# Optimization experiments

Hardware: AMD Instinct MI355X
Metric: run time of the kernel (lower is better)

Reference implementation:

```python
import jax, jax.numpy as jnp
import numpy as np

B, N, T, D = 8, 32, 49, 4
K = 4            # edge_types
HE = 256         # encoder_hidden
HD = 256         # decoder_hidden (msg_hid == msg_out == n_hid)
TEMP = 0.5
SKIP_FIRST = True
EPS = 1e-5
E = N * (N - 1)  # 992 directed edges (off-diagonal)


def setup_inputs() -> dict:
    key = jax.random.key(0)
    ks = jax.random.split(key, 32)
    it = iter(range(32))

    def lin(fi, fo):
        k = ks[next(it)]
        return (jax.random.normal(k, (fi, fo), jnp.float32) / np.sqrt(fi)).astype(jnp.float32)

    def bias(fo):
        return jnp.full((fo,), 0.1, jnp.float32)

    off = ~np.eye(N, dtype=bool)
    recv_np, send_np = np.where(off)  # rel_rec rows, rel_send cols
    recv_idx = jnp.asarray(recv_np, jnp.int32)
    send_idx = jnp.asarray(send_np, jnp.int32)

    data = jax.random.normal(ks[next(it)], (B, N, T, D), jnp.float32)
    u = jax.random.uniform(ks[next(it)], (B, E, K), jnp.float32, 1e-6, 1.0 - 1e-6)
    gumbel = -jnp.log(-jnp.log(u))

    inp = {"data": data, "gumbel": gumbel, "recv_idx": recv_idx, "send_idx": send_idx}
    # Encoder: 4 MLPs (fc1, fc2, bn gamma/beta) + fc_out
    enc_dims = [(T * D, HE), (2 * HE, HE), (HE, HE), (3 * HE, HE)]
    for i, (fi, fh) in enumerate(enc_dims, start=1):
        inp[f"e{i}_w1"] = lin(fi, HE)
        inp[f"e{i}_b1"] = bias(HE)
        inp[f"e{i}_w2"] = lin(HE, HE)
        inp[f"e{i}_b2"] = bias(HE)
        inp[f"e{i}_g"] = jnp.ones((HE,), jnp.float32)
        inp[f"e{i}_be"] = jnp.zeros((HE,), jnp.float32)
    inp["fc_w"] = lin(HE, K)
    inp["fc_b"] = bias(K)
    # Decoder: per-edge-type message MLPs (stacked) + output MLP
    inp["mw1"] = jnp.stack([lin(2 * D, HD) for _ in range(K)])
    inp["mb1"] = jnp.zeros((K, HD), jnp.float32)
    inp["mw2"] = jnp.stack([lin(HD, HD) for _ in range(K)])
    inp["mb2"] = jnp.zeros((K, HD), jnp.float32)
    inp["ow1"] = lin(D + HD, HD)
    inp["ob1"] = jnp.zeros((HD,), jnp.float32)
    inp["ow2"] = lin(HD, HD)
    inp["ob2"] = jnp.zeros((HD,), jnp.float32)
    inp["ow3"] = lin(HD, D)
    inp["ob3"] = jnp.zeros((D,), jnp.float32)
    return inp


def _mlp(x, w1, b1, w2, b2, g, be):
    # Two-layer ELU net + batch norm over all leading dims (training-mode stats).
    x = jax.nn.elu(x @ w1 + b1)
    x = jax.nn.elu(x @ w2 + b2)
    m = x.mean(axis=(0, 1), keepdims=True)
    v = x.var(axis=(0, 1), keepdims=True)
    return (x - m) / jnp.sqrt(v + EPS) * g + be


def reference(data, gumbel, recv_idx, send_idx,
              e1_w1, e1_b1, e1_w2, e1_b2, e1_g, e1_be,
              e2_w1, e2_b1, e2_w2, e2_b2, e2_g, e2_be,
              e3_w1, e3_b1, e3_w2, e3_b2, e3_g, e3_be,
              e4_w1, e4_b1, e4_w2, e4_b2, e4_g, e4_be,
              fc_w, fc_b, mw1, mb1, mw2, mb2,
              ow1, ob1, ow2, ob2, ow3, ob3):
    # ---------- Encoder ----------
    x = data.reshape(B, N, T * D)
    x = _mlp(x, e1_w1, e1_b1, e1_w2, e1_b2, e1_g, e1_be)          # [B,N,HE]
    edges = jnp.concatenate([x[:, send_idx], x[:, recv_idx]], -1)  # [B,E,2HE]
    x = _mlp(edges, e2_w1, e2_b1, e2_w2, e2_b2, e2_g, e2_be)       # [B,E,HE]
    x_skip = x
    # edge2node: rel_rec^T @ x == scatter-add by receiver, then /N
    incoming = jnp.zeros((B, N, HE), x.dtype).at[:, recv_idx, :].add(x) / N
    x = _mlp(incoming, e3_w1, e3_b1, e3_w2, e3_b2, e3_g, e3_be)    # [B,N,HE]
    edges2 = jnp.concatenate([x[:, send_idx], x[:, recv_idx]], -1)  # [B,E,2HE]
    x = jnp.concatenate([edges2, x_skip], -1)                       # [B,E,3HE]
    x = _mlp(x, e4_w1, e4_b1, e4_w2, e4_b2, e4_g, e4_be)
    logits = x @ fc_w + fc_b                                        # [B,E,K]

    rel_type = jax.nn.softmax((logits + gumbel) / TEMP, axis=-1)    # gumbel-softmax (soft)
    prob = jax.nn.softmax(logits, axis=-1)

    # ---------- Decoder (pred_steps=1) ----------
    inputs = jnp.transpose(data, (0, 2, 1, 3))                      # [B,T,N,D]
    rt = rel_type[:, None, :, :]                                    # [B,1,E,K] broadcast over T
    senders = inputs[:, :, send_idx, :]                             # [B,T,E,D]
    receivers = inputs[:, :, recv_idx, :]
    pre_msg = jnp.concatenate([senders, receivers], -1)             # [B,T,E,2D]

    start = 1 if SKIP_FIRST else 0
    all_msgs = jnp.zeros((B, T, E, HD), pre_msg.dtype)
    for k in range(start, K):
        msg = jax.nn.relu(pre_msg @ mw1[k] + mb1[k])
        msg = jax.nn.relu(msg @ mw2[k] + mb2[k])
        all_msgs = all_msgs + msg * rt[..., k:k + 1]

    # scatter-sum messages to receiving nodes
    agg = jnp.zeros((B, T, N, HD), all_msgs.dtype).at[:, :, recv_idx, :].add(all_msgs)
    aug = jnp.concatenate([inputs, agg], -1)                        # [B,T,N,D+HD]
    p = jax.nn.relu(aug @ ow1 + ob1)
    p = jax.nn.relu(p @ ow2 + ob2)
    p = p @ ow3 + ob3
    step = inputs + p                                               # [B,T,N,D]

    output = jnp.transpose(step[:, :T - 1], (0, 2, 1, 3))           # [B,N,T-1,D]
    return (output, prob)
```

## Files before the change

kernel.cpp:

```cpp
#include <hip/hip_runtime.h>
#include <hip/hip_bf16.h>

#define NNODES 32
#define TSTEPS 49
#define NEDGE  992
#define ROWS_E 7936
#define ROWS_OUT 12544
#define EPSV 1e-5f

typedef __hip_bfloat16 bf16;
typedef __attribute__((ext_vector_type(8))) short bf16x8;
typedef __attribute__((ext_vector_type(4))) float f32x4;

__device__ inline float eluf(float x){ return x > 0.f ? x : (__expf(x) - 1.f); }
__device__ inline float bfu2f(unsigned short u){ unsigned v = ((unsigned)u) << 16; return *reinterpret_cast<float*>(&v); }
__device__ inline unsigned pack_bf16(float a, float b){
  __hip_bfloat16 ha = __float2bfloat16(a), hb = __float2bfloat16(b);
  unsigned short ua = *reinterpret_cast<unsigned short*>(&ha);
  unsigned short ub = *reinterpret_cast<unsigned short*>(&hb);
  return (unsigned)ua | ((unsigned)ub << 16);
}

__global__ void prep_weights(const float* e2w1, const float* e2w2, const float* e4w1, const float* e4w2,
                             const float* mw2, const float* ow1, const float* ow2,
                             bf16* w2aT, bf16* w2bT, bf16* w4aT, bf16* w4bT,
                             bf16* mw2T, bf16* ow1T, bf16* ow2T){
  int i = blockIdx.x*256 + threadIdx.x;
  if (i < 131072){ int n = i >> 9, c = i & 511; w2aT[i] = __float2bfloat16(e2w1[c*256+n]); return; } i -= 131072;
  if (i < 65536) { int n = i >> 8, c = i & 255; w2bT[i] = __float2bfloat16(e2w2[c*256+n]); return; } i -= 65536;
  if (i < 196608){ int n = i / 768, c = i % 768; w4aT[i] = __float2bfloat16(e4w1[c*256+n]); return; } i -= 196608;
  if (i < 65536) { int n = i >> 8, c = i & 255; w4bT[i] = __float2bfloat16(e4w2[c*256+n]); return; } i -= 65536;
  if (i < 262144){ int k = i >> 16, r = i & 65535; int n = r >> 8, c = r & 255;
                   mw2T[i] = __float2bfloat16(mw2[(k*256+c)*256+n]); return; } i -= 262144;
  if (i < 73728) { int n = i / 288, c = i % 288;
                   ow1T[i] = (c < 260) ? __float2bfloat16(ow1[c*256+n]) : __float2bfloat16(0.f); return; } i -= 73728;
  if (i < 65536) { int n = i >> 8, c = i & 255; ow2T[i] = __float2bfloat16(ow2[c*256+n]); return; }
}

template<int KIN>
__global__ void small_mlp(const float* __restrict__ X, const float* __restrict__ w1, const float* __restrict__ b1,
                          const float* __restrict__ w2, const float* __restrict__ b2, float* __restrict__ H){
  __shared__ float xs[KIN];
  __shared__ float h1[256];
  int r = blockIdx.x, f = threadIdx.x;
  for (int c = f; c < KIN; c += 256) xs[c] = X[(size_t)r*KIN + c];
  __syncthreads();
  float acc = b1[f];
  for (int c = 0; c < KIN; c++) acc = fmaf(xs[c], w1[c*256+f], acc);
  h1[f] = eluf(acc);
  __syncthreads();
  float a2 = b2[f];
  for (int c = 0; c < 256; c++) a2 = fmaf(h1[c], w2[c*256+f], a2);
  H[(size_t)r*256 + f] = eluf(a2);
}

__global__ void bn_small(const float* __restrict__ H, const float* __restrict__ g, const float* __restrict__ be,
                         bf16* __restrict__ Xout){
  int f = threadIdx.x;
  float s = 0.f, s2 = 0.f;
  for (int r = 0; r < 256; r++){ float v = H[r*256+f]; s += v; s2 += v*v; }
  float m = s * (1.f/256.f), var = s2 * (1.f/256.f) - m*m;
  float sc = g[f] * rsqrtf(var + EPSV), sh = be[f] - m*sc;
  for (int r = 0; r < 256; r++) Xout[r*256+f] = __float2bfloat16(H[r*256+f]*sc + sh);
}

__global__ void gather2(const bf16* __restrict__ X, const int* __restrict__ send, const int* __restrict__ recv,
                        bf16* __restrict__ A){
  int i = blockIdx.x*256 + threadIdx.x;
  int row = i >> 6, ch = i & 63;
  int b = row / NEDGE, e = row % NEDGE;
  int c8 = ch*8;
  int src_n = (c8 < 256) ? send[e] : recv[e];
  int c = c8 & 255;
  *reinterpret_cast<uint4*>(A + (size_t)row*512 + c8) =
      *reinterpret_cast<const uint4*>(X + (size_t)(b*NNODES + src_n)*256 + c);
}

__global__ void gather3(const bf16* __restrict__ X3, const bf16* __restrict__ X2,
                        const int* __restrict__ send, const int* __restrict__ recv, bf16* __restrict__ A){
  int i = blockIdx.x*256 + threadIdx.x;
  int row = i / 96, ch = i % 96;
  int b = row / NEDGE, e = row % NEDGE;
  int c8 = ch*8;
  const bf16* src;
  if (c8 < 256)       src = X3 + (size_t)(b*NNODES + send[e])*256 + c8;
  else if (c8 < 512)  src = X3 + (size_t)(b*NNODES + recv[e])*256 + (c8-256);
  else                src = X2 + (size_t)row*256 + (c8-512);
  *reinterpret_cast<uint4*>(A + (size_t)row*768 + c8) = *reinterpret_cast<const uint4*>(src);
}

template<int K, int ACT, bool OBF>
__global__ __launch_bounds__(256,2) void gemm_mfma(const bf16* __restrict__ A, const bf16* __restrict__ WT,
                                                   const float* __restrict__ bias, void* __restrict__ Y){
  int mb = blockIdx.x;
  int tid = threadIdx.x;
  int w = tid >> 6, l = tid & 63, l15 = l & 15, lq = l >> 4;
  f32x4 acc[8][4];
  #pragma unroll
  for (int m = 0; m < 8; m++)
    #pragma unroll
    for (int nt = 0; nt < 4; nt++) acc[m][nt] = (f32x4){0.f,0.f,0.f,0.f};
  const bf16* Ab = A + (size_t)mb*128*K;
  int nw = w*64;
  for (int s = 0; s < K/32; s++){
    int c0 = s*32 + lq*8;
    bf16x8 bfr[4];
    #pragma unroll
    for (int nt = 0; nt < 4; nt++){
      int fcol = nw + nt*16 + l15;
      bfr[nt] = *reinterpret_cast<const bf16x8*>(WT + (size_t)fcol*K + c0);
    }
    #pragma unroll
    for (int m = 0; m < 8; m++){
      bf16x8 afr = *reinterpret_cast<const bf16x8*>(Ab + (size_t)(m*16 + l15)*K + c0);
      #pragma unroll
      for (int nt = 0; nt < 4; nt++)
        acc[m][nt] = __builtin_amdgcn_mfma_f32_16x16x32_bf16(afr, bfr[nt], acc[m][nt], 0, 0, 0);
    }
  }
  #pragma unroll
  for (int m = 0; m < 8; m++)
    #pragma unroll
    for (int nt = 0; nt < 4; nt++){
      int fcol = nw + nt*16 + l15;
      float bv = bias[fcol];
      #pragma unroll
      for (int v = 0; v < 4; v++){
        int row = mb*128 + m*16 + lq*4 + v;
        float val = acc[m][nt][v] + bv;
        if (ACT == 1) val = fmaxf(val, 0.f);
        else if (ACT == 2) val = eluf(val);
        if (OBF) ((bf16*)Y)[(size_t)row*256 + fcol] = __float2bfloat16(val);
        else     ((float*)Y)[(size_t)row*256 + fcol] = val;
      }
    }
}

__global__ void bn_stats(const float* __restrict__ Y, float* __restrict__ part){
  int f = threadIdx.x;
  int r0 = blockIdx.x*64;
  float s = 0.f, s2 = 0.f;
  for (int r = 0; r < 64; r++){ float v = Y[(size_t)(r0+r)*256 + f]; s += v; s2 += v*v; }
  part[blockIdx.x*512 + f] = s;
  part[blockIdx.x*512 + 256 + f] = s2;
}
__global__ void bn_finalize(const float* __restrict__ part, int nb, const float* __restrict__ g,
                            const float* __restrict__ be, float* __restrict__ prm, float nrows){
  int f = threadIdx.x;
  float s = 0.f, s2 = 0.f;
  for (int i = 0; i < nb; i++){ s += part[i*512+f]; s2 += part[i*512+256+f]; }
  float m = s / nrows, var = s2 / nrows - m*m;
  float sc = g[f] * rsqrtf(var + EPSV);
  prm[f] = sc; prm[256+f] = be[f] - m*sc;
}
__global__ void bn_apply(const float* __restrict__ Y, const float* __restrict__ prm, bf16* __restrict__ X){
  int i = blockIdx.x*256 + threadIdx.x;
  int f = i & 255;
  X[i] = __float2bfloat16(Y[i]*prm[f] + prm[256+f]);
}

__global__ void seg_incoming(const bf16* __restrict__ X2, float* __restrict__ inc){
  int bn = blockIdx.x; int b = bn >> 5, n = bn & 31;
  int f = threadIdx.x;
  const bf16* p = X2 + (size_t)(b*NEDGE + n*31)*256 + f;
  float s = 0.f;
  for (int j = 0; j < 31; j++) s += __bfloat162float(p[j*256]);
  inc[bn*256 + f] = s * (1.f/32.f);
}

__global__ void fc_softmax(const bf16* __restrict__ X4, const float* __restrict__ fcw, const float* __restrict__ fcb,
                           const float* __restrict__ gumbel, float* __restrict__ prob_out, float* __restrict__ rt){
  int r = blockIdx.x*256 + threadIdx.x;
  if (r >= ROWS_E) return;
  float l0 = fcb[0], l1 = fcb[1], l2 = fcb[2], l3 = fcb[3];
  const bf16* xr = X4 + (size_t)r*256;
  for (int c = 0; c < 256; c += 8){
    uint4 u = *reinterpret_cast<const uint4*>(xr + c);
    unsigned uu[4] = {u.x, u.y, u.z, u.w};
    #pragma unroll
    for (int q = 0; q < 4; q++){
      float x0 = bfu2f((unsigned short)(uu[q] & 0xffff));
      float x1 = bfu2f((unsigned short)(uu[q] >> 16));
      int cc = c + 2*q;
      float4 w0 = *reinterpret_cast<const float4*>(fcw + cc*4);
      float4 w1 = *reinterpret_cast<const float4*>(fcw + (cc+1)*4);
      l0 += x0*w0.x + x1*w1.x; l1 += x0*w0.y + x1*w1.y;
      l2 += x0*w0.z + x1*w1.z; l3 += x0*w0.w + x1*w1.w;
    }
  }
  float mx = fmaxf(fmaxf(l0,l1), fmaxf(l2,l3));
  float e0 = __expf(l0-mx), e1 = __expf(l1-mx), e2 = __expf(l2-mx), e3 = __expf(l3-mx);
  float inv = 1.f / (e0+e1+e2+e3);
  prob_out[(size_t)r*4+0] = e0*inv; prob_out[(size_t)r*4+1] = e1*inv;
  prob_out[(size_t)r*4+2] = e2*inv; prob_out[(size_t)r*4+3] = e3*inv;
  float4 gv = *reinterpret_cast<const float4*>(gumbel + (size_t)r*4);
  float t0 = (l0+gv.x)*2.f, t1 = (l1+gv.y)*2.f, t2 = (l2+gv.z)*2.f, t3 = (l3+gv.w)*2.f;
  float mx2 = fmaxf(fmaxf(t0,t1), fmaxf(t2,t3));
  float f0 = __expf(t0-mx2), f1 = __expf(t1-mx2), f2 = __expf(t2-mx2), f3 = __expf(t3-mx2);
  float inv2 = 1.f / (f0+f1+f2+f3);
  rt[(size_t)r*4+0] = f0*inv2; rt[(size_t)r*4+1] = f1*inv2;
  rt[(size_t)r*4+2] = f2*inv2; rt[(size_t)r*4+3] = f3*inv2;
}

__global__ __launch_bounds__(256,2) void decoder_msg(
    const float* __restrict__ data, const int* __restrict__ send,
    const float* __restrict__ rt, const float* __restrict__ mw1,
    const float* __restrict__ mb1, const bf16* __restrict__ mw2T,
    const float* __restrict__ mb2, bf16* __restrict__ Aaug){
  __shared__ __align__(16) float pm[128][8];
  __shared__ __align__(16) float rts[128][4];
  __shared__ __align__(16) float aggl[4][256];
  __shared__ __align__(16) short hA[128*256];
  int bx = blockIdx.x;
  int bt = bx >> 3, rg = bx & 7;
  int b = bt / TSTEPS, t = bt % TSTEPS;
  int n0 = rg * 4;
  int tid = threadIdx.x;
  {
    int r = tid >> 1, half = tid & 1;
    int g = r >> 5, j = r & 31;
    int n = n0 + g;
    float4 v = make_float4(0.f,0.f,0.f,0.f);
    if (j < 31){
      int e = n*31 + j;
      int src = half ? n : send[e];
      v = *reinterpret_cast<const float4*>(data + ((size_t)(b*NNODES + src)*TSTEPS + t)*4);
    }
    *reinterpret_cast<float4*>(&pm[r][half*4]) = v;
    if (half == 0){
      float4 rv = make_float4(0.f,0.f,0.f,0.f);
      if (j < 31){
        int e = n*31 + j;
        rv = *reinterpret_cast<const float4*>(rt + ((size_t)b*NEDGE + e)*4);
      }
      *reinterpret_cast<float4*>(&rts[r][0]) = rv;
    }
  }
  for (int i = tid; i < 1024; i += 256) ((float*)aggl)[i] = 0.f;
  __syncthreads();

  int w = tid >> 6, l = tid & 63, l15 = l & 15, lq = l >> 4;

  for (int kk = 1; kk < 4; kk++){
    {
      int p = tid & 127, hf = tid >> 7;
      float wv0[8], wv1[8];
      #pragma unroll
      for (int c = 0; c < 8; c++){
        float2 ww = *reinterpret_cast<const float2*>(mw1 + ((size_t)kk*8 + c)*256 + 2*p);
        wv0[c] = ww.x; wv1[c] = ww.y;
      }
      float2 bbv = *reinterpret_cast<const float2*>(mb1 + kk*256 + 2*p);
      for (int r = hf*64; r < hf*64 + 64; r++){
        float a0 = bbv.x, a1 = bbv.y;
        #pragma unroll
        for (int c = 0; c < 8; c++){ float x = pm[r][c]; a0 = fmaf(x, wv0[c], a0); a1 = fmaf(x, wv1[c], a1); }
        a0 = fmaxf(a0, 0.f); a1 = fmaxf(a1, 0.f);
        int byteoff = r*512 + ((4*p) ^ ((r & 7) << 4));
        *reinterpret_cast<unsigned*>(reinterpret_cast<char*>(hA) + byteoff) = pack_bf16(a0, a1);
      }
    }
    __syncthreads();

    f32x4 acc[8][4];
    #pragma unroll
    for (int m = 0; m < 8; m++)
      #pragma unroll
      for (int nt = 0; nt < 4; nt++) acc[m][nt] = (f32x4){0.f,0.f,0.f,0.f};
    const bf16* wk = mw2T + (size_t)kk*65536;
    for (int s = 0; s < 8; s++){
      int c0 = s*32 + lq*8;
      bf16x8 bfr[4];
      #pragma unroll
      for (int nt = 0; nt < 4; nt++){
        int fcol = w*64 + nt*16 + l15;
        bfr[nt] = *reinterpret_cast<const bf16x8*>(wk + (size_t)fcol*256 + c0);
      }
      #pragma unroll
      for (int m = 0; m < 8; m++){
        int row = m*16 + l15;
        int byteoff = row*512 + ((s*64 + lq*16) ^ ((row & 7) << 4));
        bf16x8 af = *reinterpret_cast<const bf16x8*>(reinterpret_cast<const char*>(hA) + byteoff);
        #pragma unroll
        for (int nt = 0; nt < 4; nt++)
          acc[m][nt] = __builtin_amdgcn_mfma_f32_16x16x32_bf16(af, bfr[nt], acc[m][nt], 0, 0, 0);
      }
    }
    #pragma unroll
    for (int m = 0; m < 8; m++){
      int g = m >> 1;
      #pragma unroll
      for (int nt = 0; nt < 4; nt++){
        int fcol = w*64 + nt*16 + l15;
        float bv = mb2[kk*256 + fcol];
        float ssum = 0.f;
        #pragma unroll
        for (int v = 0; v < 4; v++){
          int row = m*16 + lq*4 + v;
          float msg = fmaxf(acc[m][nt][v] + bv, 0.f);
          ssum += msg * rts[row][kk];
        }
        ssum += __shfl_xor(ssum, 16);
        ssum += __shfl_xor(ssum, 32);
        if (lq == 0) aggl[g][fcol] += ssum;
      }
    }
    __syncthreads();
  }

  for (int i = tid; i < 4*288; i += 256){
    int g = i / 288, c = i % 288;
    float val;
    if (c < 4)        val = pm[g*32][4 + c];
    else if (c < 260) val = aggl[g][c - 4];
    else              val = 0.f;
    Aaug[(size_t)(bt*NNODES + n0 + g)*288 + c] = __float2bfloat16(val);
  }
}

__global__ void final_out(const bf16* __restrict__ P2, const float* __restrict__ ow3,
                          const float* __restrict__ ob3, const float* __restrict__ data,
                          float* __restrict__ out){
  int r = blockIdx.x*256 + threadIdx.x;
  if (r >= ROWS_OUT) return;
  int bt = r >> 5, n = r & 31;
  int b = bt / TSTEPS, t = bt % TSTEPS;
  float a0 = ob3[0], a1 = ob3[1], a2 = ob3[2], a3 = ob3[3];
  const bf16* pr = P2 + (size_t)r*256;
  for (int c = 0; c < 256; c += 8){
    uint4 u = *reinterpret_cast<const uint4*>(pr + c);
    unsigned uu[4] = {u.x, u.y, u.z, u.w};
    #pragma unroll
    for (int q = 0; q < 4; q++){
      float x0 = bfu2f((unsigned short)(uu[q] & 0xffff));
      float x1 = bfu2f((unsigned short)(uu[q] >> 16));
      int cc = c + 2*q;
      float4 w0 = *reinterpret_cast<const float4*>(ow3 + cc*4);
      float4 w1 = *reinterpret_cast<const float4*>(ow3 + (cc+1)*4);
      a0 += x0*w0.x + x1*w1.x; a1 += x0*w0.y + x1*w1.y;
      a2 += x0*w0.z + x1*w1.z; a3 += x0*w0.w + x1*w1.w;
    }
  }
  if (t < TSTEPS-1){
    float4 dv = *reinterpret_cast<const float4*>(data + ((size_t)(b*NNODES + n)*TSTEPS + t)*4);
    float4 o; o.x = dv.x + a0; o.y = dv.y + a1; o.z = dv.z + a2; o.w = dv.w + a3;
    *reinterpret_cast<float4*>(out + ((size_t)(b*NNODES + n)*(TSTEPS-1) + t)*4) = o;
  }
}

extern "C" void kernel_launch(void* const* d_in, const int* in_sizes, int n_in,
                              void* d_out, int out_size, void* d_ws, size_t ws_size,
                              hipStream_t stream){
  const float* data    = (const float*)d_in[0];
  const float* gumbel  = (const float*)d_in[1];
  const int*   recv_idx= (const int*)d_in[2];
  const int*   send_idx= (const int*)d_in[3];
  const float* e1_w1=(const float*)d_in[4],  *e1_b1=(const float*)d_in[5],
             * e1_w2=(const float*)d_in[6],  *e1_b2=(const float*)d_in[7],
             * e1_g =(const float*)d_in[8],  *e1_be=(const float*)d_in[9];
  const float* e2_w1=(const float*)d_in[10], *e2_b1=(const float*)d_in[11],
             * e2_w2=(const float*)d_in[12], *e2_b2=(const float*)d_in[13],
             * e2_g =(const float*)d_in[14], *e2_be=(const float*)d_in[15];
  const float* e3_w1=(const float*)d_in[16], *e3_b1=(const float*)d_in[17],
             * e3_w2=(const float*)d_in[18], *e3_b2=(const float*)d_in[19],
             * e3_g =(const float*)d_in[20], *e3_be=(const float*)d_in[21];
  const float* e4_w1=(const float*)d_in[22], *e4_b1=(const float*)d_in[23],
             * e4_w2=(const float*)d_in[24], *e4_b2=(const float*)d_in[25],
             * e4_g =(const float*)d_in[26], *e4_be=(const float*)d_in[27];
  const float* fc_w=(const float*)d_in[28], *fc_b=(const float*)d_in[29];
  const float* mw1=(const float*)d_in[30], *mb1=(const float*)d_in[31];
  const float* mw2=(const float*)d_in[32], *mb2=(const float*)d_in[33];
  const float* ow1=(const float*)d_in[34], *ob1=(const float*)d_in[35];
  const float* ow2=(const float*)d_in[36], *ob2=(const float*)d_in[37];
  const float* ow3=(const float*)d_in[38], *ob3=(const float*)d_in[39];

  char* ws = (char*)d_ws;
  size_t off = 0;
  auto alloc = [&](size_t bytes)->void*{ void* p = ws + off; off = (off + bytes + 255) & ~(size_t)255; return p; };
  bf16* W2AT = (bf16*)alloc((size_t)131072*2);
  bf16* W2BT = (bf16*)alloc((size_t)65536*2);
  bf16* W4AT = (bf16*)alloc((size_t)196608*2);
  bf16* W4BT = (bf16*)alloc((size_t)65536*2);
  bf16* MW2T = (bf16*)alloc((size_t)262144*2);
  bf16* OW1T = (bf16*)alloc((size_t)73728*2);
  bf16* OW2T = (bf16*)alloc((size_t)65536*2);
  bf16* X1   = (bf16*)alloc((size_t)65536*2);
  float* HS  = (float*)alloc((size_t)65536*4);
  bf16* ABUF = (bf16*)alloc((size_t)7936*768*2);
  bf16* YBF  = (bf16*)alloc((size_t)12544*256*2);
  float* YF32= (float*)alloc((size_t)7936*256*4);
  bf16* X2   = (bf16*)alloc((size_t)7936*256*2);
  bf16* X3   = (bf16*)alloc((size_t)65536*2);
  bf16* X4   = (bf16*)alloc((size_t)7936*256*2);
  bf16* P2   = (bf16*)alloc((size_t)12544*256*2);
  float* INC = (float*)alloc((size_t)65536*4);
  float* RT  = (float*)alloc((size_t)7936*4*4);
  float* PART= (float*)alloc((size_t)124*512*4);
  float* PRM = (float*)alloc((size_t)512*4);

  float* out = (float*)d_out;
  float* prob_out = out + 49152;

  prep_weights<<<3360,256,0,stream>>>(e2_w1,e2_w2,e4_w1,e4_w2,mw2,ow1,ow2,
                                      W2AT,W2BT,W4AT,W4BT,MW2T,OW1T,OW2T);
  small_mlp<196><<<256,256,0,stream>>>(data, e1_w1,e1_b1,e1_w2,e1_b2, HS);
  bn_small<<<1,256,0,stream>>>(HS, e1_g, e1_be, X1);
  gather2<<<1984,256,0,stream>>>(X1, send_idx, recv_idx, ABUF);
  gemm_mfma<512,2,true><<<62,256,0,stream>>>(ABUF, W2AT, e2_b1, YBF);
  gemm_mfma<256,2,false><<<62,256,0,stream>>>(YBF, W2BT, e2_b2, YF32);
  bn_stats<<<124,256,0,stream>>>(YF32, PART);
  bn_finalize<<<1,256,0,stream>>>(PART, 124, e2_g, e2_be, PRM, 7936.f);
  bn_apply<<<7936,256,0,stream>>>(YF32, PRM, X2);
  seg_incoming<<<256,256,0,stream>>>(X2, INC);
  small_mlp<256><<<256,256,0,stream>>>(INC, e3_w1,e3_b1,e3_w2,e3_b2, HS);
  bn_small<<<1,256,0,stream>>>(HS, e3_g, e3_be, X3);
  gather3<<<2976,256,0,stream>>>(X3, X2, send_idx, recv_idx, ABUF);
  gemm_mfma<768,2,true><<<62,256,0,stream>>>(ABUF, W4AT, e4_b1, YBF);
  gemm_mfma<256,2,false><<<62,256,0,stream>>>(YBF, W4BT, e4_b2, YF32);
  bn_stats<<<124,256,0,stream>>>(YF32, PART);
  bn_finalize<<<1,256,0,stream>>>(PART, 124, e4_g, e4_be, PRM, 7936.f);
  bn_apply<<<7936,256,0,stream>>>(YF32, PRM, X4);
  fc_softmax<<<31,256,0,stream>>>(X4, fc_w, fc_b, gumbel, prob_out, RT);
  decoder_msg<<<3136,256,0,stream>>>(data, send_idx, RT, mw1, mb1, MW2T, mb2, ABUF);
  gemm_mfma<288,1,true><<<98,256,0,stream>>>(ABUF, OW1T, ob1, YBF);
  gemm_mfma<256,1,true><<<98,256,0,stream>>>(YBF, OW2T, ob2, P2);
  final_out<<<49,256,0,stream>>>(P2, ow3, ob3, data, out);
}
```

Before: 655.8 us.

## Precompute per-node first-layer message projections and shrink decoder/GEMM row tiles

The first message-MLP layer is split algebraically into sender and receiver projections that are computed once per node and timestep by a new dec_sr kernel. decoder_msg then gathers and adds these bf16 vectors with relu instead of recomputing the 8-input layer for every edge. decoder_msg blocks now cover 2 receivers (64 rows) instead of 4, and all gemm_mfma launches use 64-row tiles with doubled grids and launch_bounds of 4 waves per EU, to fill more CUs. In exchange it writes and reads extra S/R buffers (about 38 MB in bf16) and rounds the first-layer pre-activations to bf16 before the add.

After: 873.5 us. +33.2%, slower.

```diff
diff --git a/kernel.cpp b/kernel.cpp
--- a/kernel.cpp
+++ b/kernel.cpp
@@ -6,6 +6,7 @@
 #define NEDGE  992
 #define ROWS_E 7936
 #define ROWS_OUT 12544
+#define BNT 12544
 #define EPSV 1e-5f
 
 typedef __hip_bfloat16 bf16;
@@ -14,11 +15,19 @@
 
 __device__ inline float eluf(float x){ return x > 0.f ? x : (__expf(x) - 1.f); }
 __device__ inline float bfu2f(unsigned short u){ unsigned v = ((unsigned)u) << 16; return *reinterpret_cast<float*>(&v); }
-__device__ inline unsigned pack_bf16(float a, float b){
-  __hip_bfloat16 ha = __float2bfloat16(a), hb = __float2bfloat16(b);
-  unsigned short ua = *reinterpret_cast<unsigned short*>(&ha);
-  unsigned short ub = *reinterpret_cast<unsigned short*>(&hb);
-  return (unsigned)ua | ((unsigned)ub << 16);
+
+__device__ inline bf16x8 addrelu_pack(bf16x8 s, bf16x8 r){
+  bf16x8 out;
+  #pragma unroll
+  for (int i = 0; i < 8; i++){
+    unsigned ss = ((unsigned)(unsigned short)s[i]) << 16;
+    unsigned rr = ((unsigned)(unsigned short)r[i]) << 16;
+    float v = *reinterpret_cast<float*>(&ss) + *reinterpret_cast<float*>(&rr);
+    v = fmaxf(v, 0.f);
+    __hip_bfloat16 h = __float2bfloat16(v);
+    out[i] = *reinterpret_cast<short*>(&h);
+  }
+  return out;
 }
 
 __global__ void prep_weights(const float* e2w1, const float* e2w2, const float* e4w1, const float* e4w2,
@@ -35,6 +44,26 @@
   if (i < 73728) { int n = i / 288, c = i % 288;
                    ow1T[i] = (c < 260) ? __float2bfloat16(ow1[c*256+n]) : __float2bfloat16(0.f); return; } i -= 73728;
   if (i < 65536) { int n = i >> 8, c = i & 255; ow2T[i] = __float2bfloat16(ow2[c*256+n]); return; }
+}
+
+__global__ void dec_sr(const float* __restrict__ data, const float* __restrict__ mw1,
+                       const float* __restrict__ mb1, bf16* __restrict__ Sb, bf16* __restrict__ Rb){
+  int blk = blockIdx.x;
+  int c = threadIdx.x;
+  float4 xv = *reinterpret_cast<const float4*>(data + (size_t)blk*4);
+  float x[4] = {xv.x, xv.y, xv.z, xv.w};
+  #pragma unroll
+  for (int kk = 1; kk < 4; kk++){
+    float s = mb1[kk*256 + c], r = 0.f;
+    #pragma unroll
+    for (int d = 0; d < 4; d++){
+      s = fmaf(x[d], mw1[((size_t)(kk*8 + d))*256 + c], s);
+      r = fmaf(x[d], mw1[((size_t)(kk*8 + 4 + d))*256 + c], r);
+    }
+    size_t o = ((size_t)(kk-1)*BNT + blk)*256 + c;
+    Sb[o] = __float2bfloat16(s);
+    Rb[o] = __float2bfloat16(r);
+  }
 }
 
 template<int KIN>
@@ -89,18 +118,18 @@
   *reinterpret_cast<uint4*>(A + (size_t)row*768 + c8) = *reinterpret_cast<const uint4*>(src);
 }
 
-template<int K, int ACT, bool OBF>
-__global__ __launch_bounds__(256,2) void gemm_mfma(const bf16* __restrict__ A, const bf16* __restrict__ WT,
+template<int K, int ACT, bool OBF, int MT>
+__global__ __launch_bounds__(256,4) void gemm_mfma(const bf16* __restrict__ A, const bf16* __restrict__ WT,
                                                    const float* __restrict__ bias, void* __restrict__ Y){
   int mb = blockIdx.x;
   int tid = threadIdx.x;
   int w = tid >> 6, l = tid & 63, l15 = l & 15, lq = l >> 4;
-  f32x4 acc[8][4];
+  f32x4 acc[MT/16][4];
   #pragma unroll
-  for (int m = 0; m < 8; m++)
+  for (int m = 0; m < MT/16; m++)
     #pragma unroll
     for (int nt = 0; nt < 4; nt++) acc[m][nt] = (f32x4){0.f,0.f,0.f,0.f};
-  const bf16* Ab = A + (size_t)mb*128*K;
+  const bf16* Ab = A + (size_t)mb*MT*K;
   int nw = w*64;
   for (int s = 0; s < K/32; s++){
     int c0 = s*32 + lq*8;
@@ -111,7 +140,7 @@
       bfr[nt] = *reinterpret_cast<const bf16x8*>(WT + (size_t)fcol*K + c0);
     }
     #pragma unroll
-    for (int m = 0; m < 8; m++){
+    for (int m = 0; m < MT/16; m++){
       bf16x8 afr = *reinterpret_cast<const bf16x8*>(Ab + (size_t)(m*16 + l15)*K + c0);
       #pragma unroll
       for (int nt = 0; nt < 4; nt++)
@@ -119,14 +148,14 @@
     }
   }
   #pragma unroll
-  for (int m = 0; m < 8; m++)
+  for (int m = 0; m < MT/16; m++)
     #pragma unroll
     for (int nt = 0; nt < 4; nt++){
       int fcol = nw + nt*16 + l15;
       float bv = bias[fcol];
       #pragma unroll
       for (int v = 0; v < 4; v++){
-        int row = mb*128 + m*16 + lq*4 + v;
+        int row = mb*MT + m*16 + lq*4 + v;
         float val = acc[m][nt][v] + bv;
         if (ACT == 1) val = fmaxf(val, 0.f);
         else if (ACT == 2) val = eluf(val);
@@ -202,69 +231,65 @@
   rt[(size_t)r*4+2] = f2*inv2; rt[(size_t)r*4+3] = f3*inv2;
 }
 
-__global__ __launch_bounds__(256,2) void decoder_msg(
+__global__ __launch_bounds__(256,4) void decoder_msg(
     const float* __restrict__ data, const int* __restrict__ send,
-    const float* __restrict__ rt, const float* __restrict__ mw1,
-    const float* __restrict__ mb1, const bf16* __restrict__ mw2T,
-    const float* __restrict__ mb2, bf16* __restrict__ Aaug){
-  __shared__ __align__(16) float pm[128][8];
-  __shared__ __align__(16) float rts[128][4];
-  __shared__ __align__(16) float aggl[4][256];
-  __shared__ __align__(16) short hA[128*256];
+    const float* __restrict__ rt, const bf16* __restrict__ Sb, const bf16* __restrict__ Rb,
+    const bf16* __restrict__ mw2T, const float* __restrict__ mb2, bf16* __restrict__ Aaug){
+  __shared__ __align__(16) short hA[64*256];
+  __shared__ __align__(16) float rts[64][4];
+  __shared__ __align__(16) float aggl[2][256];
+  __shared__ int sendn[64];
   int bx = blockIdx.x;
-  int bt = bx >> 3, rg = bx & 7;
+  int bt = bx >> 4, rg = bx & 15;
   int b = bt / TSTEPS, t = bt % TSTEPS;
-  int n0 = rg * 4;
+  int n0 = rg * 2;
   int tid = threadIdx.x;
-  {
-    int r = tid >> 1, half = tid & 1;
-    int g = r >> 5, j = r & 31;
-    int n = n0 + g;
-    float4 v = make_float4(0.f,0.f,0.f,0.f);
+  if (tid < 64){
+    int r = tid;
+    int n = n0 + (r >> 5), j = r & 31;
     if (j < 31){
       int e = n*31 + j;
-      int src = half ? n : send[e];
-      v = *reinterpret_cast<const float4*>(data + ((size_t)(b*NNODES + src)*TSTEPS + t)*4);
-    }
-    *reinterpret_cast<float4*>(&pm[r][half*4]) = v;
-    if (half == 0){
-      float4 rv = make_float4(0.f,0.f,0.f,0.f);
-      if (j < 31){
-        int e = n*31 + j;
-        rv = *reinterpret_cast<const float4*>(rt + ((size_t)b*NEDGE + e)*4);
-      }
-      *reinterpret_cast<float4*>(&rts[r][0]) = rv;
-    }
-  }
-  for (int i = tid; i < 1024; i += 256) ((float*)aggl)[i] = 0.f;
+      sendn[r] = send[e];
+      *reinterpret_cast<float4*>(&rts[r][0]) = *reinterpret_cast<const float4*>(rt + ((size_t)b*NEDGE + e)*4);
+    } else {
+      sendn[r] = 0;
+      *reinterpret_cast<float4*>(&rts[r][0]) = make_float4(0.f,0.f,0.f,0.f);
+    }
+  }
+  for (int i = tid; i < 512; i += 256) ((float*)aggl)[i] = 0.f;
   __syncthreads();
 
   int w = tid >> 6, l = tid & 63, l15 = l & 15, lq = l >> 4;
+  int row = tid & 63, q = tid >> 6;
+  int nrecv = n0 + (row >> 5);
+  bool valid = (row & 31) < 31;
 
   for (int kk = 1; kk < 4; kk++){
     {
-      int p = tid & 127, hf = tid >> 7;
-      float wv0[8], wv1[8];
-      #pragma unroll
-      for (int c = 0; c < 8; c++){
-        float2 ww = *reinterpret_cast<const float2*>(mw1 + ((size_t)kk*8 + c)*256 + 2*p);
-        wv0[c] = ww.x; wv1[c] = ww.y;
+      int sn = sendn[row];
+      size_t sbase = ((size_t)(kk-1)*BNT + (size_t)((b*NNODES + sn)*TSTEPS + t))*256;
+      size_t rbase = ((size_t)(kk-1)*BNT + (size_t)((b*NNODES + nrecv)*TSTEPS + t))*256;
+      #pragma unroll
+      for (int f = 0; f < 8; f++){
+        int chunk = q + 4*f;
+        int c0 = chunk*8;
+        bf16x8 pk;
+        if (valid){
+          bf16x8 s8 = *reinterpret_cast<const bf16x8*>(Sb + sbase + c0);
+          bf16x8 r8 = *reinterpret_cast<const bf16x8*>(Rb + rbase + c0);
+          pk = addrelu_pack(s8, r8);
+        } else {
+          pk = (bf16x8){0,0,0,0,0,0,0,0};
+        }
+        int byteoff = row*512 + ((chunk*16) ^ ((row & 7) << 4));
+        *reinterpret_cast<bf16x8*>(reinterpret_cast<char*>(hA) + byteoff) = pk;
       }
-      float2 bbv = *reinterpret_cast<const float2*>(mb1 + kk*256 + 2*p);
-      for (int r = hf*64; r < hf*64 + 64; r++){
-        float a0 = bbv.x, a1 = bbv.y;
-        #pragma unroll
-        for (int c = 0; c < 8; c++){ float x = pm[r][c]; a0 = fmaf(x, wv0[c], a0); a1 = fmaf(x, wv1[c], a1); }
-        a0 = fmaxf(a0, 0.f); a1 = fmaxf(a1, 0.f);
-        int byteoff = r*512 + ((4*p) ^ ((r & 7) << 4));
-        *reinterpret_cast<unsigned*>(reinterpret_cast<char*>(hA) + byteoff) = pack_bf16(a0, a1);
-      }
     }
     __syncthreads();
 
-    f32x4 acc[8][4];
-    #pragma unroll
-    for (int m = 0; m < 8; m++)
+    f32x4 acc[4][4];
+    #pragma unroll
+    for (int m = 0; m < 4; m++)
       #pragma unroll
       for (int nt = 0; nt < 4; nt++) acc[m][nt] = (f32x4){0.f,0.f,0.f,0.f};
     const bf16* wk = mw2T + (size_t)kk*65536;
@@ -277,9 +302,9 @@
         bfr[nt] = *reinterpret_cast<const bf16x8*>(wk + (size_t)fcol*256 + c0);
       }
       #pragma unroll
-      for (int m = 0; m < 8; m++){
-        int row = m*16 + l15;
-        int byteoff = row*512 + ((s*64 + lq*16) ^ ((row & 7) << 4));
+      for (int m = 0; m < 4; m++){
+        int rowm = m*16 + l15;
+        int byteoff = rowm*512 + ((s*64 + lq*16) ^ ((rowm & 7) << 4));
         bf16x8 af = *reinterpret_cast<const bf16x8*>(reinterpret_cast<const char*>(hA) + byteoff);
         #pragma unroll
         for (int nt = 0; nt < 4; nt++)
@@ -287,8 +312,7 @@
       }
     }
     #pragma unroll
-    for (int m = 0; m < 8; m++){
-      int g = m >> 1;
+    for (int m = 0; m < 4; m++){
       #pragma unroll
       for (int nt = 0; nt < 4; nt++){
         int fcol = w*64 + nt*16 + l15;
@@ -296,22 +320,22 @@
         float ssum = 0.f;
         #pragma unroll
         for (int v = 0; v < 4; v++){
-          int row = m*16 + lq*4 + v;
+          int rowa = m*16 + lq*4 + v;
           float msg = fmaxf(acc[m][nt][v] + bv, 0.f);
-          ssum += msg * rts[row][kk];
+          ssum += msg * rts[rowa][kk];
         }
         ssum += __shfl_xor(ssum, 16);
         ssum += __shfl_xor(ssum, 32);
-        if (lq == 0) aggl[g][fcol] += ssum;
+        if (lq == 0) aggl[m >> 1][fcol] += ssum;
       }
     }
     __syncthreads();
   }
 
-  for (int i = tid; i < 4*288; i += 256){
+  for (int i = tid; i < 2*288; i += 256){
     int g = i / 288, c = i % 288;
     float val;
-    if (c < 4)        val = pm[g*32][4 + c];
+    if (c < 4)        val = data[((size_t)(b*NNODES + n0 + g)*TSTEPS + t)*4 + c];
     else if (c < 260) val = aggl[g][c - 4];
     else              val = 0.f;
     Aaug[(size_t)(bt*NNODES + n0 + g)*288 + c] = __float2bfloat16(val);
@@ -397,17 +421,21 @@
   float* RT  = (float*)alloc((size_t)7936*4*4);
   float* PART= (float*)alloc((size_t)124*512*4);
   float* PRM = (float*)alloc((size_t)512*4);
+  bf16* SBUF = (bf16*)alloc((size_t)3*BNT*256*2);
+  bf16* RBUF = (bf16*)alloc((size_t)3*BNT*256*2);
+  bf16* AAUG = (bf16*)alloc((size_t)12544*288*2);
 
   float* out = (float*)d_out;
   float* prob_out = out + 49152;
 
   prep_weights<<<3360,256,0,stream>>>(e2_w1,e2_w2,e4_w1,e4_w2,mw2,ow1,ow2,
                                       W2AT,W2BT,W4AT,W4BT,MW2T,OW1T,OW2T);
+  dec_sr<<<BNT,256,0,stream>>>(data, mw1, mb1, SBUF, RBUF);
   small_mlp<196><<<256,256,0,stream>>>(data, e1_w1,e1_b1,e1_w2,e1_b2, HS);
   bn_small<<<1,256,0,stream>>>(HS, e1_g, e1_be, X1);
   gather2<<<1984,256,0,stream>>>(X1, send_idx, recv_idx, ABUF);
-  gemm_mfma<512,2,true><<<62,256,0,stream>>>(ABUF, W2AT, e2_b1, YBF);
-  gemm_mfma<256,2,false><<<62,256,0,stream>>>(YBF, W2BT, e2_b2, YF32);
+  gemm_mfma<512,2,true,64><<<124,256,0,stream>>>(ABUF, W2AT, e2_b1, YBF);
+  gemm_mfma<256,2,false,64><<<124,256,0,stream>>>(YBF, W2BT, e2_b2, YF32);
   bn_stats<<<124,256,0,stream>>>(YF32, PART);
   bn_finalize<<<1,256,0,stream>>>(PART, 124, e2_g, e2_be, PRM, 7936.f);
   bn_apply<<<7936,256,0,stream>>>(YF32, PRM, X2);
@@ -415,14 +443,14 @@
   small_mlp<256><<<256,256,0,stream>>>(INC, e3_w1,e3_b1,e3_w2,e3_b2, HS);
   bn_small<<<1,256,0,stream>>>(HS, e3_g, e3_be, X3);
   gather3<<<2976,256,0,stream>>>(X3, X2, send_idx, recv_idx, ABUF);
-  gemm_mfma<768,2,true><<<62,256,0,stream>>>(ABUF, W4AT, e4_b1, YBF);
-  gemm_mfma<256,2,false><<<62,256,0,stream>>>(YBF, W4BT, e4_b2, YF32);
+  gemm_mfma<768,2,true,64><<<124,256,0,stream>>>(ABUF, W4AT, e4_b1, YBF);
+  gemm_mfma<256,2,false,64><<<124,256,0,stream>>>(YBF, W4BT, e4_b2, YF32);
   bn_stats<<<124,256,0,stream>>>(YF32, PART);
   bn_finalize<<<1,256,0,stream>>>(PART, 124, e4_g, e4_be, PRM, 7936.f);
   bn_apply<<<7936,256,0,stream>>>(YF32, PRM, X4);
   fc_softmax<<<31,256,0,stream>>>(X4, fc_w, fc_b, gumbel, prob_out, RT);
-  decoder_msg<<<3136,256,0,stream>>>(data, send_idx, RT, mw1, mb1, MW2T, mb2, ABUF);
-  gemm_mfma<288,1,true><<<98,256,0,stream>>>(ABUF, OW1T, ob1, YBF);
-  gemm_mfma<256,1,true><<<98,256,0,stream>>>(YBF, OW2T, ob2, P2);
+  decoder_msg<<<6272,256,0,stream>>>(data, send_idx, RT, SBUF, RBUF, MW2T, mb2, AAUG);
+  gemm_mfma<288,1,true,64><<<196,256,0,stream>>>(AAUG, OW1T, ob1, YBF);
+  gemm_mfma<256,1,true,64><<<196,256,0,stream>>>(YBF, OW2T, ob2, P2);
   final_out<<<49,256,0,stream>>>(P2, ow3, ob3, data, out);
 }
```
